# Kernel tuning notes

Hardware: AMD Instinct MI355X
Metric: run time of the kernel (lower is better)

The kernel has to match this reference:

```python
import jax, jax.numpy as jnp
import numpy as np

B, T, C, H = 4, 2048, 768, 12
D = C // H
EPS = 1e-5


def layernorm(x, g, b):
    mu = jnp.mean(x, axis=-1, keepdims=True)
    var = jnp.mean(jnp.square(x - mu), axis=-1, keepdims=True)
    return (x - mu) * jax.lax.rsqrt(var + EPS) * g + b


def setup_inputs() -> dict:
    key = jax.random.key(0)
    ks = jax.random.split(key, 16)
    s = 0.02
    return {
        "x": jax.random.normal(ks[0], (B, T, C), jnp.float32),
        "Wq": jax.random.normal(ks[1], (C, C), jnp.float32) * s,
        "bq": jnp.zeros((C,), jnp.float32),
        "Wk": jax.random.normal(ks[2], (C, C), jnp.float32) * s,
        "bk": jnp.zeros((C,), jnp.float32),
        "Wv": jax.random.normal(ks[3], (C, C), jnp.float32) * s,
        "bv": jnp.zeros((C,), jnp.float32),
        "Wo": jax.random.normal(ks[4], (C, C), jnp.float32) * s,
        "bo": jnp.zeros((C,), jnp.float32),
        "g1": jnp.ones((C,), jnp.float32),
        "b1": jnp.zeros((C,), jnp.float32),
        "g2": jnp.ones((C,), jnp.float32),
        "b2": jnp.zeros((C,), jnp.float32),
        "W1": jax.random.normal(ks[5], (C, 4 * C), jnp.float32) * s,
        "bm1": jnp.zeros((4 * C,), jnp.float32),
        "W2": jax.random.normal(ks[6], (4 * C, C), jnp.float32) * s,
        "bm2": jnp.zeros((C,), jnp.float32),
    }


def reference(x, Wq, bq, Wk, bk, Wv, bv, Wo, bo, g1, b1, g2, b2, W1, bm1, W2, bm2):
    # --- attention branch ---
    h = layernorm(x, g1, b1)
    q = (h @ Wq + bq).reshape(B, T, H, D)
    k = (h @ Wk + bk).reshape(B, T, H, D)
    v = (h @ Wv + bv).reshape(B, T, H, D)
    att = jnp.einsum('bqhd,bkhd->bhqk', q, k) / jnp.sqrt(jnp.float32(D))
    causal = jnp.tril(jnp.ones((T, T), bool))
    att = jnp.where(causal, att, -jnp.inf)
    att = jax.nn.softmax(att, axis=-1)
    o = jnp.einsum('bhqk,bkhd->bqhd', att, v).reshape(B, T, C)
    x = x + o @ Wo + bo
    # --- MLP branch ---
    h = layernorm(x, g2, b2)
    h = jax.nn.gelu(h @ W1 + bm1, approximate=False)
    return x + h @ W2 + bm2
```

## Files before the change

kernel.cpp:

```cpp
#include <hip/hip_runtime.h>
#include <hip/hip_bf16.h>

#define B_ 4
#define T_ 2048
#define C_ 768
#define H_ 12
#define D_ 64
#define QS_ 2304

typedef __attribute__((ext_vector_type(8))) short short8;
typedef __attribute__((ext_vector_type(4))) short short4v;
typedef __attribute__((ext_vector_type(4))) float f32x4;

__device__ __forceinline__ unsigned short f2bf(float f) {
    __hip_bfloat16 h = __float2bfloat16(f);
    return *reinterpret_cast<unsigned short*>(&h);
}

__device__ __forceinline__ float bf2f(unsigned short u) {
    return __bfloat162float(*reinterpret_cast<const __hip_bfloat16*>(&u));
}

__device__ __forceinline__ unsigned cvt_pk_bf16(float lo, float hi) {
    unsigned r;
    asm("v_cvt_pk_bf16_f32 %0, %1, %2" : "=v"(r) : "v"(lo), "v"(hi));
    return r;
}

__device__ __forceinline__ void gl_lds16(const void* g, void* l) {
    __builtin_amdgcn_global_load_lds((const __attribute__((address_space(1))) unsigned int*)g,
                                     (__attribute__((address_space(3))) unsigned int*)l,
                                     16, 0, 0);
}

__device__ __forceinline__ void transpose_dev(const float* __restrict__ W,
                                              unsigned short* __restrict__ Wt,
                                              int K, int N, int bx, int by,
                                              float (*t)[65]) {
    int n0 = bx * 64, k0 = by * 64;
    int r = threadIdx.x >> 4, c4 = (threadIdx.x & 15) * 4;
    #pragma unroll
    for (int i = 0; i < 4; ++i) {
        float4 v = *(const float4*)(W + (size_t)(k0 + i * 16 + r) * N + n0 + c4);
        t[i*16 + r][c4 + 0] = v.x;
        t[i*16 + r][c4 + 1] = v.y;
        t[i*16 + r][c4 + 2] = v.z;
        t[i*16 + r][c4 + 3] = v.w;
    }
    __syncthreads();
    #pragma unroll
    for (int i = 0; i < 4; ++i) {
        ushort4 o;
        o.x = f2bf(t[c4 + 0][i*16 + r]);
        o.y = f2bf(t[c4 + 1][i*16 + r]);
        o.z = f2bf(t[c4 + 2][i*16 + r]);
        o.w = f2bf(t[c4 + 3][i*16 + r]);
        *(ushort4*)(Wt + (size_t)(n0 + i * 16 + r) * K + k0 + c4) = o;
    }
}

__global__ __launch_bounds__(256) void prep_all(const float* __restrict__ Wq,
                                                const float* __restrict__ Wk,
                                                const float* __restrict__ Wv,
                                                const float* __restrict__ Wo,
                                                const float* __restrict__ W1,
                                                const float* __restrict__ W2,
                                                const float* __restrict__ bq,
                                                const float* __restrict__ bk,
                                                const float* __restrict__ bv,
                                                const float* __restrict__ x,
                                                const float* __restrict__ g1,
                                                const float* __restrict__ b1,
                                                unsigned short* __restrict__ wqkvt,
                                                unsigned short* __restrict__ wot,
                                                unsigned short* __restrict__ w1t,
                                                unsigned short* __restrict__ w2t,
                                                float* __restrict__ bqkv,
                                                unsigned short* __restrict__ ln1h) {
    __shared__ float t[64][65];
    __shared__ float ws[8];
    int blk = blockIdx.x;
    int tid = threadIdx.x;

    if (blk < 576) {
        int which = blk / 144, idx = blk % 144;
        const float* src = (which == 0) ? Wq : (which == 1) ? Wk : (which == 2) ? Wv : Wo;
        unsigned short* dst = (which == 3) ? wot : wqkvt + (size_t)which * C_ * C_;
        transpose_dev(src, dst, C_, C_, idx % 12, idx / 12, t);
    } else if (blk < 1152) {
        int idx = blk - 576;
        transpose_dev(W1, w1t, C_, 4 * C_, idx % 48, idx / 48, t);
    } else if (blk < 1728) {
        int idx = blk - 1152;
        transpose_dev(W2, w2t, 4 * C_, C_, idx % 12, idx / 12, t);
    } else if (blk < 1737) {
        int i = (blk - 1728) * 256 + tid;
        bqkv[i] = (i < 768) ? bq[i] : (i < 1536) ? bk[i - 768] : bv[i - 1536];
    } else {
        int row = blk - 1737;
        const float* xr = x + (size_t)row * C_;
        float v0 = xr[tid], v1 = xr[tid + 256], v2 = xr[tid + 512];
        float s = v0 + v1 + v2;
        #pragma unroll
        for (int off = 1; off < 64; off <<= 1) s += __shfl_xor(s, off);
        int wid = tid >> 6, lane = tid & 63;
        if (lane == 0) ws[wid] = s;
        __syncthreads();
        float mean = (ws[0] + ws[1] + ws[2] + ws[3]) * (1.0f / C_);
        float d0 = v0 - mean, d1 = v1 - mean, d2 = v2 - mean;
        float qs = d0*d0 + d1*d1 + d2*d2;
        #pragma unroll
        for (int off = 1; off < 64; off <<= 1) qs += __shfl_xor(qs, off);
        if (lane == 0) ws[4 + wid] = qs;
        __syncthreads();
        float var = (ws[4] + ws[5] + ws[6] + ws[7]) * (1.0f / C_);
        float rs = rsqrtf(var + 1e-5f);
        unsigned short* orow = ln1h + (size_t)row * C_;
        orow[tid]       = f2bf(d0 * rs * g1[tid]       + b1[tid]);
        orow[tid + 256] = f2bf(d1 * rs * g1[tid + 256] + b1[tid + 256]);
        orow[tid + 512] = f2bf(d2 * rs * g1[tid + 512] + b1[tid + 512]);
    }
}

__global__ __launch_bounds__(256) void ln_bf16_bf16(const unsigned short* __restrict__ x,
                                                    const float* __restrict__ g,
                                                    const float* __restrict__ b,
                                                    unsigned short* __restrict__ out) {
    int row = blockIdx.x;
    int tid = threadIdx.x;
    const unsigned short* xr = x + (size_t)row * C_;
    float v0 = bf2f(xr[tid]), v1 = bf2f(xr[tid + 256]), v2 = bf2f(xr[tid + 512]);
    float s = v0 + v1 + v2;
    #pragma unroll
    for (int off = 1; off < 64; off <<= 1) s += __shfl_xor(s, off);
    __shared__ float ws1[4], ws2[4];
    int wid = tid >> 6, lane = tid & 63;
    if (lane == 0) ws1[wid] = s;
    __syncthreads();
    float mean = (ws1[0] + ws1[1] + ws1[2] + ws1[3]) * (1.0f / C_);
    float d0 = v0 - mean, d1 = v1 - mean, d2 = v2 - mean;
    float qs = d0*d0 + d1*d1 + d2*d2;
    #pragma unroll
    for (int off = 1; off < 64; off <<= 1) qs += __shfl_xor(qs, off);
    if (lane == 0) ws2[wid] = qs;
    __syncthreads();
    float var = (ws2[0] + ws2[1] + ws2[2] + ws2[3]) * (1.0f / C_);
    float rs = rsqrtf(var + 1e-5f);
    unsigned short* orow = out + (size_t)row * C_;
    orow[tid]       = f2bf(d0 * rs * g[tid]       + b[tid]);
    orow[tid + 256] = f2bf(d1 * rs * g[tid + 256] + b[tid + 256]);
    orow[tid + 512] = f2bf(d2 * rs * g[tid + 512] + b[tid + 512]);
}

template <int EPI>
__global__ __launch_bounds__(256) void gemm_bf16(const unsigned short* __restrict__ A,
                                                 const unsigned short* __restrict__ Bt,
                                                 const float* __restrict__ bias,
                                                 const void* __restrict__ resid,
                                                 void* __restrict__ Cout,
                                                 unsigned short* __restrict__ aux,
                                                 int M, int N, int K, int gx) {
    __shared__ short As[2][128 * 32];
    __shared__ short Bs[2][128 * 32];
    int tid = threadIdx.x;
    int w = tid >> 6, l = tid & 63;
    int nb = gridDim.x;
    int per = nb >> 3;
    int fid = (int)blockIdx.x;
    int wid = (fid & 7) * per + (fid >> 3);
    int bn = wid % gx, bm = wid / gx;
    int wr = w >> 1, wc = w & 1;

    f32x4 acc[4][4];
    #pragma unroll
    for (int m = 0; m < 4; ++m)
        #pragma unroll
        for (int n = 0; n < 4; ++n)
            acc[m][n] = (f32x4){0.f, 0.f, 0.f, 0.f};

    const short* Ag = (const short*)A + (size_t)(bm * 128) * K;
    const short* Bg = (const short*)Bt + (size_t)(bn * 128) * K;
    int srow = tid >> 2;
    int scol = (tid & 3) * 8;
    int lrow = l & 15, lk = (l >> 4) * 8;

    auto stage = [&](int buf, int k0) {
        #pragma unroll
        for (int i = 0; i < 2; ++i) {
            gl_lds16(Ag + (size_t)(i * 64 + srow) * K + k0 + scol,
                     (char*)&As[buf][0] + i * 4096 + w * 1024);
            gl_lds16(Bg + (size_t)(i * 64 + srow) * K + k0 + scol,
                     (char*)&Bs[buf][0] + i * 4096 + w * 1024);
        }
    };

    int nk = K / 32;
    stage(0, 0);
    __syncthreads();

    for (int kt = 0; kt < nk; ++kt) {
        int cur = kt & 1;
        if (kt + 1 < nk) stage(cur ^ 1, (kt + 1) * 32);

        short8 av[4], bv[4];
        #pragma unroll
        for (int m = 0; m < 4; ++m)
            av[m] = *(const short8*)&As[cur][(wr * 64 + m * 16 + lrow) * 32 + lk];
        #pragma unroll
        for (int n = 0; n < 4; ++n)
            bv[n] = *(const short8*)&Bs[cur][(wc * 64 + n * 16 + lrow) * 32 + lk];
        #pragma unroll
        for (int m = 0; m < 4; ++m)
            #pragma unroll
            for (int n = 0; n < 4; ++n)
                acc[m][n] = __builtin_amdgcn_mfma_f32_16x16x32_bf16(av[m], bv[n], acc[m][n], 0, 0, 0);

        __syncthreads();
    }

    int lcol = l & 15, lr4 = (l >> 4) * 4;
    int row0 = bm * 128 + wr * 64;
    int col0 = bn * 128 + wc * 64;
    #pragma unroll
    for (int m = 0; m < 4; ++m) {
        #pragma unroll
        for (int n = 0; n < 4; ++n) {
            int col = col0 + n * 16 + lcol;
            float bz = bias[col];
            if (EPI == 5 && col0 >= 1536) {
                ushort4 o4;
                o4.x = f2bf(acc[m][n][0] + bz);
                o4.y = f2bf(acc[m][n][1] + bz);
                o4.z = f2bf(acc[m][n][2] + bz);
                o4.w = f2bf(acc[m][n][3] + bz);
                int row = row0 + m * 16 + lr4;
                int c = col - 1536;
                *(ushort4*)(aux + ((size_t)(row >> 11) * 768 + c) * (size_t)T_ + (row & 2047)) = o4;
            } else {
                #pragma unroll
                for (int r = 0; r < 4; ++r) {
                    int row = row0 + m * 16 + lr4 + r;
                    float v = acc[m][n][r] + bz;
                    if (EPI == 1) {
                        float u = fmaf(0.044715f * v, v * v, v);
                        float e = __builtin_amdgcn_exp2f(u * -2.3022127f);
                        v = v * __builtin_amdgcn_rcpf(1.0f + e);
                        ((unsigned short*)Cout)[(size_t)row * N + col] = f2bf(v);
                    } else if (EPI == 6) {
                        v += bf2f(((const unsigned short*)resid)[(size_t)row * N + col]);
                        ((float*)Cout)[(size_t)row * N + col] = v;
                    } else if (EPI == 7) {
                        v += ((const float*)resid)[(size_t)row * N + col];
                        ((unsigned short*)Cout)[(size_t)row * N + col] = f2bf(v);
                    } else {
                        ((unsigned short*)Cout)[(size_t)row * N + col] = f2bf(v);
                    }
                }
            }
        }
    }
}

__global__ __launch_bounds__(256) void attn_v9(const unsigned short* __restrict__ QKV,
                                               const unsigned short* __restrict__ vT,
                                               unsigned short* __restrict__ O) {
    __shared__ short Ks[128 * 64];
    __shared__ short Vt[64 * 128];

    int tid = threadIdx.x;
    int w = tid >> 6, l = tid & 63;
    int g = l >> 4, lc = l & 15;
    int wid = (int)(blockIdx.x & 7) * 192 + (int)(blockIdx.x >> 3);
    int bh = wid >> 5;
    int a  = 31 - (wid & 31);
    int b = bh / H_, h = bh % H_;
    const size_t bT = (size_t)b * T_;
    const unsigned short* Qp = QKV + h * D_;
    const unsigned short* Kp = QKV + 768 + h * D_;
    const unsigned short* vTb = vT + ((size_t)b * 768 + h * 64) * (size_t)T_;
    const float SCL = 0.125f * 1.44269504088896340736f;

    int qw = a * 64 + w * 16;

    short8 qf[2];
    {
        const unsigned short* qp = Qp + (bT + qw + lc) * QS_;
        qf[0] = *(const short8*)(qp + g * 8);
        qf[1] = *(const short8*)(qp + 32 + g * 8);
    }

    f32x4 oacc[4];
    #pragma unroll
    for (int n = 0; n < 4; ++n) oacc[n] = (f32x4){0.f, 0.f, 0.f, 0.f};
    float mrun = 4.0f, lpart = 0.f;

    int ntiles = (a >> 1) + 1;
    for (int kt = 0; kt < ntiles; ++kt) {
        int k0 = kt * 128;
        if (kt) __syncthreads();

        #pragma unroll
        for (int c = 0; c < 4; ++c) {
            int row = w * 32 + c * 8 + (l >> 3);
            int inner = (l & 7) * 16;
            const char* src = (const char*)(Kp + (bT + k0 + row) * QS_)
                              + (inner ^ ((row & 7) << 4));
            gl_lds16(src, (char*)Ks + w * 4096 + c * 1024);
        }
        #pragma unroll
        for (int c = 0; c < 4; ++c) {
            int d = w * 16 + c * 4 + (l >> 4);
            int inner = (l & 15) * 16;
            const char* src = (const char*)(vTb + (size_t)d * T_ + k0)
                              + (inner ^ ((d & 7) << 4));
            gl_lds16(src, (char*)Vt + w * 4096 + c * 1024);
        }
        __syncthreads();

        uint2 qd[8];
        float lmaxP[4] = {-INFINITY, -INFINITY, -INFINITY, -INFINITY};
        float rsumP[4] = {0.f, 0.f, 0.f, 0.f};
        bool full = (k0 + 127 <= qw);
        #pragma unroll
        for (int mk = 0; mk < 8; ++mk) {
            f32x4 s = (f32x4){0.f, 0.f, 0.f, 0.f};
            __builtin_amdgcn_s_setprio(1);
            #pragma unroll
            for (int ksd = 0; ksd < 2; ++ksd) {
                int row = mk * 16 + lc;
                int byt = (row * 128 + ksd * 64 + g * 16) ^ ((row & 7) << 4);
                short8 av = *(const short8*)((char*)Ks + byt);
                s = __builtin_amdgcn_mfma_f32_16x16x32_bf16(av, qf[ksd], s, 0, 0, 0);
            }
            __builtin_amdgcn_s_setprio(0);
            float p[4];
            #pragma unroll
            for (int r = 0; r < 4; ++r) {
                float sv = s[r] * SCL;
                if (!full && (k0 + mk * 16 + g * 4 + r > qw + lc)) sv = -INFINITY;
                lmaxP[r] = fmaxf(lmaxP[r], sv);
                float pv = __builtin_amdgcn_exp2f(sv - mrun);
                p[r] = pv;
                rsumP[r] += pv;
            }
            qd[mk].x = cvt_pk_bf16(p[0], p[1]);
            qd[mk].y = cvt_pk_bf16(p[2], p[3]);
        }
        float lmax = fmaxf(fmaxf(lmaxP[0], lmaxP[1]), fmaxf(lmaxP[2], lmaxP[3]));
        lpart += (rsumP[0] + rsumP[1]) + (rsumP[2] + rsumP[3]);

        #pragma unroll
        for (int ks = 0; ks < 4; ++ks) {
            uint2 qa = qd[ks * 2], qb = qd[ks * 2 + 1];
            int srcLo = lc + ((g & 1) << 5);
            int srcHi = srcLo + 16;
            unsigned a0 = (unsigned)__shfl((int)qa.x, srcLo);
            unsigned a1 = (unsigned)__shfl((int)qa.y, srcLo);
            unsigned a2 = (unsigned)__shfl((int)qa.x, srcHi);
            unsigned a3 = (unsigned)__shfl((int)qa.y, srcHi);
            unsigned b0 = (unsigned)__shfl((int)qb.x, srcLo);
            unsigned b1 = (unsigned)__shfl((int)qb.y, srcLo);
            unsigned b2 = (unsigned)__shfl((int)qb.x, srcHi);
            unsigned b3 = (unsigned)__shfl((int)qb.y, srcHi);
            bool lo = (g < 2);
            union { unsigned u[4]; short8 s8; } pa;
            pa.u[0] = lo ? a0 : b0;
            pa.u[1] = lo ? a1 : b1;
            pa.u[2] = lo ? a2 : b2;
            pa.u[3] = lo ? a3 : b3;
            short8 vbv[4];
            #pragma unroll
            for (int n = 0; n < 4; ++n) {
                int row = n * 16 + lc;
                int byt = (row * 256 + ks * 64 + g * 16) ^ ((row & 7) << 4);
                vbv[n] = *(const short8*)((char*)Vt + byt);
            }
            __builtin_amdgcn_s_setprio(1);
            #pragma unroll
            for (int n = 0; n < 4; ++n)
                oacc[n] = __builtin_amdgcn_mfma_f32_16x16x32_bf16(pa.s8, vbv[n], oacc[n], 0, 0, 0);
            __builtin_amdgcn_s_setprio(0);
        }

        if (__any(lmax > mrun + 8.0f)) {
            lmax = fmaxf(lmax, __shfl_xor(lmax, 16));
            lmax = fmaxf(lmax, __shfl_xor(lmax, 32));
            float mnew = fmaxf(mrun, lmax);
            float cc = __builtin_amdgcn_exp2f(mrun - mnew);
            lpart *= cc;
            mrun = mnew;
            #pragma unroll
            for (int r = 0; r < 4; ++r) {
                float cr = __shfl(cc, (l & 48) + g * 4 + r);
                #pragma unroll
                for (int n = 0; n < 4; ++n) oacc[n][r] *= cr;
            }
        }
    }

    float lv = lpart;
    lv += __shfl_xor(lv, 16);
    lv += __shfl_xor(lv, 32);
    float linv = 1.0f / lv;
    float inv[4];
    #pragma unroll
    for (int r = 0; r < 4; ++r) inv[r] = __shfl(linv, (l & 48) + g * 4 + r);
    #pragma unroll
    for (int n = 0; n < 4; ++n) {
        int col = h * D_ + n * 16 + lc;
        #pragma unroll
        for (int r = 0; r < 4; ++r) {
            int row = qw + g * 4 + r;
            O[(bT + row) * C_ + col] = f2bf(oacc[n][r] * inv[r]);
        }
    }
}

extern "C" void kernel_launch(void* const* d_in, const int* in_sizes, int n_in,
                              void* d_out, int out_size, void* d_ws, size_t ws_size,
                              hipStream_t stream) {
    const float* x   = (const float*)d_in[0];
    const float* Wq  = (const float*)d_in[1];
    const float* bq  = (const float*)d_in[2];
    const float* Wk  = (const float*)d_in[3];
    const float* bk  = (const float*)d_in[4];
    const float* Wv  = (const float*)d_in[5];
    const float* bv  = (const float*)d_in[6];
    const float* Wo  = (const float*)d_in[7];
    const float* bo  = (const float*)d_in[8];
    const float* g1  = (const float*)d_in[9];
    const float* b1  = (const float*)d_in[10];
    const float* g2  = (const float*)d_in[11];
    const float* b2  = (const float*)d_in[12];
    const float* W1  = (const float*)d_in[13];
    const float* bm1 = (const float*)d_in[14];
    const float* W2  = (const float*)d_in[15];
    const float* bm2 = (const float*)d_in[16];
    float* out = (float*)d_out;

    const size_t S = (size_t)B_ * T_ * C_;
    char* base = (char*)d_ws;
    unsigned short* ln1h = (unsigned short*)base;
    unsigned short* qkvb = (unsigned short*)(base + 2 * S);
    unsigned short* o    = ln1h;
    unsigned short* ln2h = qkvb;
    unsigned short* vT   = (unsigned short*)(base + 8 * S);
    unsigned short* hid  = (unsigned short*)(base + 4 * S);
    unsigned short* xmid = (unsigned short*)(base + 12 * S);
    unsigned short* wqkvt = (unsigned short*)(base + 16 * S);
    unsigned short* wot   = wqkvt + (size_t)3 * C_ * C_;
    unsigned short* w1t   = wot + (size_t)C_ * C_;
    unsigned short* w2t   = w1t + (size_t)C_ * 4 * C_;
    float* bqkv           = (float*)(w2t + (size_t)C_ * 4 * C_);

    const int M = B_ * T_;
    dim3 blk(256);

    prep_all<<<dim3(1737 + M), blk, 0, stream>>>(Wq, Wk, Wv, Wo, W1, W2,
                                                 bq, bk, bv, x, g1, b1,
                                                 wqkvt, wot, w1t, w2t, bqkv, ln1h);

    gemm_bf16<5><<<dim3((QS_ / 128) * (M / 128)), blk, 0, stream>>>(ln1h, wqkvt, bqkv, nullptr, qkvb, vT, M, QS_, C_, QS_ / 128);

    attn_v9<<<dim3(B_ * H_ * 32), blk, 0, stream>>>(qkvb, vT, o);

    gemm_bf16<7><<<dim3((C_ / 128) * (M / 128)), blk, 0, stream>>>(o, wot, bo, x, xmid, nullptr, M, C_, C_, C_ / 128);
    ln_bf16_bf16<<<dim3(M), blk, 0, stream>>>(xmid, g2, b2, ln2h);
    gemm_bf16<1><<<dim3((4 * C_ / 128) * (M / 128)), blk, 0, stream>>>(ln2h, w1t, bm1, nullptr, hid, nullptr, M, 4 * C_, C_, 4 * C_ / 128);
    gemm_bf16<6><<<dim3((C_ / 128) * (M / 128)), blk, 0, stream>>>(hid, w2t, bm2, xmid, out, nullptr, M, C_, 4 * C_, C_ / 128);
}
```

Before: 295.8 us.

## Process two 16-row query tiles per wave in attention to reuse K/V tiles

Each attention block now covers 128 query rows instead of 64, with every wave computing two 16-row query tiles that share the same K and V LDS fragments. This halves the grid and the number of K/V tile loads per query, and raises MFMA work per LDS read. In exchange it doubles the accumulator and probability registers, which may lower occupancy. With half as many blocks, the causal load imbalance across blocks is also coarser.

```diff
diff --git a/kernel.cpp b/kernel.cpp
--- a/kernel.cpp
+++ b/kernel.cpp
@@ -261,18 +261,18 @@
     }
 }
 
-__global__ __launch_bounds__(256) void attn_v9(const unsigned short* __restrict__ QKV,
-                                               const unsigned short* __restrict__ vT,
-                                               unsigned short* __restrict__ O) {
+__global__ __launch_bounds__(256) void attn_v11(const unsigned short* __restrict__ QKV,
+                                                const unsigned short* __restrict__ vT,
+                                                unsigned short* __restrict__ O) {
     __shared__ short Ks[128 * 64];
     __shared__ short Vt[64 * 128];
 
     int tid = threadIdx.x;
     int w = tid >> 6, l = tid & 63;
     int g = l >> 4, lc = l & 15;
-    int wid = (int)(blockIdx.x & 7) * 192 + (int)(blockIdx.x >> 3);
-    int bh = wid >> 5;
-    int a  = 31 - (wid & 31);
+    int wid = (int)(blockIdx.x & 7) * 96 + (int)(blockIdx.x >> 3);
+    int bh = wid >> 4;
+    int a  = 15 - (wid & 15);
     int b = bh / H_, h = bh % H_;
     const size_t bT = (size_t)b * T_;
     const unsigned short* Qp = QKV + h * D_;
@@ -280,21 +280,29 @@
     const unsigned short* vTb = vT + ((size_t)b * 768 + h * 64) * (size_t)T_;
     const float SCL = 0.125f * 1.44269504088896340736f;
 
-    int qw = a * 64 + w * 16;
-
-    short8 qf[2];
+    int qw1 = a * 128 + w * 32;
+    int qw2 = qw1 + 16;
+
+    short8 qf1[2], qf2[2];
     {
-        const unsigned short* qp = Qp + (bT + qw + lc) * QS_;
-        qf[0] = *(const short8*)(qp + g * 8);
-        qf[1] = *(const short8*)(qp + 32 + g * 8);
-    }
-
-    f32x4 oacc[4];
-    #pragma unroll
-    for (int n = 0; n < 4; ++n) oacc[n] = (f32x4){0.f, 0.f, 0.f, 0.f};
-    float mrun = 4.0f, lpart = 0.f;
-
-    int ntiles = (a >> 1) + 1;
+        const unsigned short* qp1 = Qp + (bT + qw1 + lc) * QS_;
+        qf1[0] = *(const short8*)(qp1 + g * 8);
+        qf1[1] = *(const short8*)(qp1 + 32 + g * 8);
+        const unsigned short* qp2 = Qp + (bT + qw2 + lc) * QS_;
+        qf2[0] = *(const short8*)(qp2 + g * 8);
+        qf2[1] = *(const short8*)(qp2 + 32 + g * 8);
+    }
+
+    f32x4 oacc1[4], oacc2[4];
+    #pragma unroll
+    for (int n = 0; n < 4; ++n) {
+        oacc1[n] = (f32x4){0.f, 0.f, 0.f, 0.f};
+        oacc2[n] = (f32x4){0.f, 0.f, 0.f, 0.f};
+    }
+    float mrun1 = 4.0f, lpart1 = 0.f;
+    float mrun2 = 4.0f, lpart2 = 0.f;
+
+    int ntiles = a + 1;
     for (int kt = 0; kt < ntiles; ++kt) {
         int k0 = kt * 128;
         if (kt) __syncthreads();
@@ -317,57 +325,90 @@
         }
         __syncthreads();
 
-        uint2 qd[8];
-        float lmaxP[4] = {-INFINITY, -INFINITY, -INFINITY, -INFINITY};
-        float rsumP[4] = {0.f, 0.f, 0.f, 0.f};
-        bool full = (k0 + 127 <= qw);
+        uint2 qd1[8], qd2[8];
+        float lmax1P[4] = {-INFINITY, -INFINITY, -INFINITY, -INFINITY};
+        float rsum1P[4] = {0.f, 0.f, 0.f, 0.f};
+        float lmax2P[4] = {-INFINITY, -INFINITY, -INFINITY, -INFINITY};
+        float rsum2P[4] = {0.f, 0.f, 0.f, 0.f};
+        bool full1 = (k0 + 127 <= qw1);
+        bool full2 = (k0 + 127 <= qw2);
         #pragma unroll
         for (int mk = 0; mk < 8; ++mk) {
-            f32x4 s = (f32x4){0.f, 0.f, 0.f, 0.f};
+            int row = mk * 16 + lc;
+            int byt0 = (row * 128 + g * 16) ^ ((row & 7) << 4);
+            short8 av0 = *(const short8*)((char*)Ks + byt0);
+            short8 av1 = *(const short8*)((char*)Ks + (byt0 ^ 64));
+            f32x4 s1 = (f32x4){0.f, 0.f, 0.f, 0.f};
+            f32x4 s2 = (f32x4){0.f, 0.f, 0.f, 0.f};
             __builtin_amdgcn_s_setprio(1);
-            #pragma unroll
-            for (int ksd = 0; ksd < 2; ++ksd) {
-                int row = mk * 16 + lc;
-                int byt = (row * 128 + ksd * 64 + g * 16) ^ ((row & 7) << 4);
-                short8 av = *(const short8*)((char*)Ks + byt);
-                s = __builtin_amdgcn_mfma_f32_16x16x32_bf16(av, qf[ksd], s, 0, 0, 0);
-            }
+            s1 = __builtin_amdgcn_mfma_f32_16x16x32_bf16(av0, qf1[0], s1, 0, 0, 0);
+            s1 = __builtin_amdgcn_mfma_f32_16x16x32_bf16(av1, qf1[1], s1, 0, 0, 0);
+            s2 = __builtin_amdgcn_mfma_f32_16x16x32_bf16(av0, qf2[0], s2, 0, 0, 0);
+            s2 = __builtin_amdgcn_mfma_f32_16x16x32_bf16(av1, qf2[1], s2, 0, 0, 0);
             __builtin_amdgcn_s_setprio(0);
-            float p[4];
+            float p1[4], p2[4];
             #pragma unroll
             for (int r = 0; r < 4; ++r) {
-                float sv = s[r] * SCL;
-                if (!full && (k0 + mk * 16 + g * 4 + r > qw + lc)) sv = -INFINITY;
-                lmaxP[r] = fmaxf(lmaxP[r], sv);
-                float pv = __builtin_amdgcn_exp2f(sv - mrun);
-                p[r] = pv;
-                rsumP[r] += pv;
-            }
-            qd[mk].x = cvt_pk_bf16(p[0], p[1]);
-            qd[mk].y = cvt_pk_bf16(p[2], p[3]);
-        }
-        float lmax = fmaxf(fmaxf(lmaxP[0], lmaxP[1]), fmaxf(lmaxP[2], lmaxP[3]));
-        lpart += (rsumP[0] + rsumP[1]) + (rsumP[2] + rsumP[3]);
+                int kk = k0 + mk * 16 + g * 4 + r;
+                float sv1 = s1[r] * SCL;
+                if (!full1 && (kk > qw1 + lc)) sv1 = -INFINITY;
+                lmax1P[r] = fmaxf(lmax1P[r], sv1);
+                float pv1 = __builtin_amdgcn_exp2f(sv1 - mrun1);
+                p1[r] = pv1;
+                rsum1P[r] += pv1;
+                float sv2 = s2[r] * SCL;
+                if (!full2 && (kk > qw2 + lc)) sv2 = -INFINITY;
+                lmax2P[r] = fmaxf(lmax2P[r], sv2);
+                float pv2 = __builtin_amdgcn_exp2f(sv2 - mrun2);
+                p2[r] = pv2;
+                rsum2P[r] += pv2;
+            }
+            qd1[mk].x = cvt_pk_bf16(p1[0], p1[1]);
+            qd1[mk].y = cvt_pk_bf16(p1[2], p1[3]);
+            qd2[mk].x = cvt_pk_bf16(p2[0], p2[1]);
+            qd2[mk].y = cvt_pk_bf16(p2[2], p2[3]);
+        }
+        float lmax1 = fmaxf(fmaxf(lmax1P[0], lmax1P[1]), fmaxf(lmax1P[2], lmax1P[3]));
+        float lmax2 = fmaxf(fmaxf(lmax2P[0], lmax2P[1]), fmaxf(lmax2P[2], lmax2P[3]));
+        lpart1 += (rsum1P[0] + rsum1P[1]) + (rsum1P[2] + rsum1P[3]);
+        lpart2 += (rsum2P[0] + rsum2P[1]) + (rsum2P[2] + rsum2P[3]);
 
         #pragma unroll
         for (int ks = 0; ks < 4; ++ks) {
-            uint2 qa = qd[ks * 2], qb = qd[ks * 2 + 1];
             int srcLo = lc + ((g & 1) << 5);
             int srcHi = srcLo + 16;
-            unsigned a0 = (unsigned)__shfl((int)qa.x, srcLo);
-            unsigned a1 = (unsigned)__shfl((int)qa.y, srcLo);
-            unsigned a2 = (unsigned)__shfl((int)qa.x, srcHi);
-            unsigned a3 = (unsigned)__shfl((int)qa.y, srcHi);
-            unsigned b0 = (unsigned)__shfl((int)qb.x, srcLo);
-            unsigned b1 = (unsigned)__shfl((int)qb.y, srcLo);
-            unsigned b2 = (unsigned)__shfl((int)qb.x, srcHi);
-            unsigned b3 = (unsigned)__shfl((int)qb.y, srcHi);
             bool lo = (g < 2);
-            union { unsigned u[4]; short8 s8; } pa;
-            pa.u[0] = lo ? a0 : b0;
-            pa.u[1] = lo ? a1 : b1;
-            pa.u[2] = lo ? a2 : b2;
-            pa.u[3] = lo ? a3 : b3;
+            union { unsigned u[4]; short8 s8; } pa1, pa2;
+            {
+                uint2 qa = qd1[ks * 2], qb = qd1[ks * 2 + 1];
+                unsigned a0 = (unsigned)__shfl((int)qa.x, srcLo);
+                unsigned a1 = (unsigned)__shfl((int)qa.y, srcLo);
+                unsigned a2 = (unsigned)__shfl((int)qa.x, srcHi);
+                unsigned a3 = (unsigned)__shfl((int)qa.y, srcHi);
+                unsigned b0 = (unsigned)__shfl((int)qb.x, srcLo);
+                unsigned b1 = (unsigned)__shfl((int)qb.y, srcLo);
+                unsigned b2 = (unsigned)__shfl((int)qb.x, srcHi);
+                unsigned b3 = (unsigned)__shfl((int)qb.y, srcHi);
+                pa1.u[0] = lo ? a0 : b0;
+                pa1.u[1] = lo ? a1 : b1;
+                pa1.u[2] = lo ? a2 : b2;
+                pa1.u[3] = lo ? a3 : b3;
+            }
+            {
+                uint2 qa = qd2[ks * 2], qb = qd2[ks * 2 + 1];
+                unsigned a0 = (unsigned)__shfl((int)qa.x, srcLo);
+                unsigned a1 = (unsigned)__shfl((int)qa.y, srcLo);
+                unsigned a2 = (unsigned)__shfl((int)qa.x, srcHi);
+                unsigned a3 = (unsigned)__shfl((int)qa.y, srcHi);
+                unsigned b0 = (unsigned)__shfl((int)qb.x, srcLo);
+                unsigned b1 = (unsigned)__shfl((int)qb.y, srcLo);
+                unsigned b2 = (unsigned)__shfl((int)qb.x, srcHi);
+                unsigned b3 = (unsigned)__shfl((int)qb.y, srcHi);
+                pa2.u[0] = lo ? a0 : b0;
+                pa2.u[1] = lo ? a1 : b1;
+                pa2.u[2] = lo ? a2 : b2;
+                pa2.u[3] = lo ? a3 : b3;
+            }
             short8 vbv[4];
             #pragma unroll
             for (int n = 0; n < 4; ++n) {
@@ -377,41 +418,77 @@
             }
             __builtin_amdgcn_s_setprio(1);
             #pragma unroll
-            for (int n = 0; n < 4; ++n)
-                oacc[n] = __builtin_amdgcn_mfma_f32_16x16x32_bf16(pa.s8, vbv[n], oacc[n], 0, 0, 0);
+            for (int n = 0; n < 4; ++n) {
+                oacc1[n] = __builtin_amdgcn_mfma_f32_16x16x32_bf16(pa1.s8, vbv[n], oacc1[n], 0, 0, 0);
+                oacc2[n] = __builtin_amdgcn_mfma_f32_16x16x32_bf16(pa2.s8, vbv[n], oacc2[n], 0, 0, 0);
+            }
             __builtin_amdgcn_s_setprio(0);
         }
 
-        if (__any(lmax > mrun + 8.0f)) {
-            lmax = fmaxf(lmax, __shfl_xor(lmax, 16));
-            lmax = fmaxf(lmax, __shfl_xor(lmax, 32));
-            float mnew = fmaxf(mrun, lmax);
-            float cc = __builtin_amdgcn_exp2f(mrun - mnew);
-            lpart *= cc;
-            mrun = mnew;
+        if (__any(lmax1 > mrun1 + 8.0f)) {
+            lmax1 = fmaxf(lmax1, __shfl_xor(lmax1, 16));
+            lmax1 = fmaxf(lmax1, __shfl_xor(lmax1, 32));
+            float mnew = fmaxf(mrun1, lmax1);
+            float cc = __builtin_amdgcn_exp2f(mrun1 - mnew);
+            lpart1 *= cc;
+            mrun1 = mnew;
             #pragma unroll
             for (int r = 0; r < 4; ++r) {
                 float cr = __shfl(cc, (l & 48) + g * 4 + r);
                 #pragma unroll
-                for (int n = 0; n < 4; ++n) oacc[n][r] *= cr;
-            }
-        }
-    }
-
-    float lv = lpart;
-    lv += __shfl_xor(lv, 16);
-    lv += __shfl_xor(lv, 32);
-    float linv = 1.0f / lv;
-    float inv[4];
-    #pragma unroll
-    for (int r = 0; r < 4; ++r) inv[r] = __shfl(linv, (l & 48) + g * 4 + r);
-    #pragma unroll
-    for (int n = 0; n < 4; ++n) {
-        int col = h * D_ + n * 16 + lc;
-        #pragma unroll
-        for (int r = 0; r < 4; ++r) {
-            int row = qw + g * 4 + r;
-            O[(bT + row) * C_ + col] = f2bf(oacc[n][r] * inv[r]);
+                for (int n = 0; n < 4; ++n) oacc1[n][r] *= cr;
+            }
+        }
+        if (__any(lmax2 > mrun2 + 8.0f)) {
+            lmax2 = fmaxf(lmax2, __shfl_xor(lmax2, 16));
+            lmax2 = fmaxf(lmax2, __shfl_xor(lmax2, 32));
+            float mnew = fmaxf(mrun2, lmax2);
+            float cc = __builtin_amdgcn_exp2f(mrun2 - mnew);
+            lpart2 *= cc;
+            mrun2 = mnew;
+            #pragma unroll
+            for (int r = 0; r < 4; ++r) {
+                float cr = __shfl(cc, (l & 48) + g * 4 + r);
+                #pragma unroll
+                for (int n = 0; n < 4; ++n) oacc2[n][r] *= cr;
+            }
+        }
+    }
+
+    {
+        float lv = lpart1;
+        lv += __shfl_xor(lv, 16);
+        lv += __shfl_xor(lv, 32);
+        float linv = 1.0f / lv;
+        float inv[4];
+        #pragma unroll
+        for (int r = 0; r < 4; ++r) inv[r] = __shfl(linv, (l & 48) + g * 4 + r);
+        #pragma unroll
+        for (int n = 0; n < 4; ++n) {
+            int col = h * D_ + n * 16 + lc;
+            #pragma unroll
+            for (int r = 0; r < 4; ++r) {
+                int row = qw1 + g * 4 + r;
+                O[(bT + row) * C_ + col] = f2bf(oacc1[n][r] * inv[r]);
+            }
+        }
+    }
+    {
+        float lv = lpart2;
+        lv += __shfl_xor(lv, 16);
+        lv += __shfl_xor(lv, 32);
+        float linv = 1.0f / lv;
+        float inv[4];
+        #pragma unroll
+        for (int r = 0; r < 4; ++r) inv[r] = __shfl(linv, (l & 48) + g * 4 + r);
+        #pragma unroll
+        for (int n = 0; n < 4; ++n) {
+            int col = h * D_ + n * 16 + lc;
+            #pragma unroll
+            for (int r = 0; r < 4; ++r) {
+                int row = qw2 + g * 4 + r;
+                O[(bT + row) * C_ + col] = f2bf(oacc2[n][r] * inv[r]);
+            }
         }
     }
 }
@@ -462,7 +539,7 @@
 
     gemm_bf16<5><<<dim3((QS_ / 128) * (M / 128)), blk, 0, stream>>>(ln1h, wqkvt, bqkv, nullptr, qkvb, vT, M, QS_, C_, QS_ / 128);
 
-    attn_v9<<<dim3(B_ * H_ * 32), blk, 0, stream>>>(qkvb, vT, o);
+    attn_v11<<<dim3(B_ * H_ * 16), blk, 0, stream>>>(qkvb, vT, o);
 
     gemm_bf16<7><<<dim3((C_ / 128) * (M / 128)), blk, 0, stream>>>(o, wot, bo, x, xmid, nullptr, M, C_, C_, C_ / 128);
     ln_bf16_bf16<<<dim3(M), blk, 0, stream>>>(xmid, g2, b2, ln2h);
```

Result: slower. 351.6 us (+18.9%).
